# Kernel optimization log

Hardware: AMD Instinct MI355X
Metric: run time of the kernel (lower is better)

Reference implementation:

```python
import jax, jax.numpy as jnp
import numpy as np

B, S, D, DQK, DV = 4, 2048, 1024, 128, 256
EPS = 1e-8


def setup_inputs() -> dict:
    key = jax.random.key(0)
    ks = jax.random.split(key, 11)
    s = lambda fan_in: 1.0 / np.sqrt(fan_in)
    return {
        "X": jax.random.normal(ks[0], (B, S, D), dtype=jnp.float32),
        "Wq": jax.random.uniform(ks[1], (D, DQK), minval=-s(D), maxval=s(D), dtype=jnp.float32),
        "bq": jax.random.uniform(ks[2], (DQK,), minval=-s(D), maxval=s(D), dtype=jnp.float32),
        "Wk": jax.random.uniform(ks[3], (D, DQK), minval=-s(D), maxval=s(D), dtype=jnp.float32),
        "bk": jax.random.uniform(ks[4], (DQK,), minval=-s(D), maxval=s(D), dtype=jnp.float32),
        "Wv": jax.random.uniform(ks[5], (D, DV), minval=-s(D), maxval=s(D), dtype=jnp.float32),
        "bv": jax.random.uniform(ks[6], (DV,), minval=-s(D), maxval=s(D), dtype=jnp.float32),
        "Wg": jax.random.uniform(ks[7], (D, DV), minval=-s(D), maxval=s(D), dtype=jnp.float32),
        "bg": jax.random.uniform(ks[8], (DV,), minval=-s(D), maxval=s(D), dtype=jnp.float32),
        "Wp": jax.random.uniform(ks[9], (DV, D), minval=-s(DV), maxval=s(DV), dtype=jnp.float32),
        "bp": jax.random.uniform(ks[10], (D,), minval=-s(DV), maxval=s(DV), dtype=jnp.float32),
    }


def _shepards(Q, K, V, p=2, eps=EPS):
    # Euclidean cdist via ||q||^2 + ||k||^2 - 2 q.k  (then sqrt)
    q2 = jnp.sum(Q * Q, axis=-1, keepdims=True)          # [B,Sq,1]
    k2 = jnp.sum(K * K, axis=-1, keepdims=True)          # [B,Sk,1]
    d2 = q2 + jnp.swapaxes(k2, -1, -2) - 2.0 * jnp.einsum("bqd,bkd->bqk", Q, K)
    Dm = jnp.sqrt(jnp.maximum(d2, 0.0))                  # [B,Sq,Sk]
    W = jnp.power(jnp.maximum(Dm, eps), -float(p))
    A = W / jnp.sum(W, axis=2, keepdims=True)
    return jnp.einsum("bqk,bkv->bqv", A, V)


def reference(X, Wq, bq, Wk, bk, Wv, bv, Wg, bg, Wp, bp):
    N = X  # norm is Identity
    Q = N @ Wq + bq
    K = N @ Wk + bk
    V = N @ Wv + bv
    A = _shepards(Q, K, V)
    G = N @ Wg + bg
    return X + (A * G) @ Wp + bp
```

## Files before the change

kernel.cpp:

```cpp
#include <hip/hip_runtime.h>
#include <stdint.h>

#define SLEN 2048
#define NROWS 8192

typedef __attribute__((ext_vector_type(4))) float f32x4;
typedef __attribute__((ext_vector_type(8))) short bf16x8;

__device__ __forceinline__ short f2bf(float f) {
  uint32_t u = __builtin_bit_cast(uint32_t, f);
  u += 0x7FFFu + ((u >> 16) & 1u);
  return (short)(u >> 16);
}
__device__ __forceinline__ float bf2f(short s) {
  uint32_t u = ((uint32_t)(uint16_t)s) << 16;
  return __builtin_bit_cast(float, u);
}
__device__ __forceinline__ f32x4 mfma16(bf16x8 a, bf16x8 b, f32x4 c) {
  return __builtin_amdgcn_mfma_f32_16x16x32_bf16(a, b, c, 0, 0, 0);
}
__device__ __forceinline__ void gld_lds16(const void* g, void* l) {
  __builtin_amdgcn_global_load_lds(
      (const __attribute__((address_space(1))) void*)g,
      (__attribute__((address_space(3))) void*)l, 16, 0, 0);
}

__global__ __launch_bounds__(256) void k_prep(
    const float* __restrict__ X,
    const float* __restrict__ Wq, const float* __restrict__ bq,
    const float* __restrict__ Wk, const float* __restrict__ bk,
    const float* __restrict__ Wv, const float* __restrict__ bv,
    const float* __restrict__ Wg, const float* __restrict__ bg,
    const float* __restrict__ Wp,
    short* __restrict__ Xb, short* __restrict__ WcatT,
    short* __restrict__ WpT, float* __restrict__ bcat) {
  int blk = blockIdx.x, tid = threadIdx.x;
  if (blk < 4096) {
    size_t e = ((size_t)blk * 256 + tid) * 8;
    f32x4 a = *(const f32x4*)&X[e];
    f32x4 b = *(const f32x4*)&X[e + 4];
    bf16x8 o;
    o[0] = f2bf(a[0]); o[1] = f2bf(a[1]); o[2] = f2bf(a[2]); o[3] = f2bf(a[3]);
    o[4] = f2bf(b[0]); o[5] = f2bf(b[1]); o[6] = f2bf(b[2]); o[7] = f2bf(b[3]);
    *(bf16x8*)&Xb[e] = o;
  } else if (blk < 7168) {
    int flat = (blk - 4096) * 256 + tid;
    int c = flat >> 10, d = flat & 1023;
    float v;
    if (c < 128)      v = Wq[d * 128 + c];
    else if (c < 256) v = Wk[d * 128 + (c - 128)];
    else if (c < 512) v = Wv[d * 256 + (c - 256)];
    else              v = Wg[d * 256 + (c - 512)];
    WcatT[flat] = f2bf(v);
  } else if (blk < 8192) {
    int flat = (blk - 7168) * 256 + tid;
    int n = flat >> 8, k = flat & 255;
    WpT[flat] = f2bf(Wp[(size_t)k * 1024 + n]);
  } else {
    int c = (blk - 8192) * 256 + tid;
    if (c < 768) {
      float v;
      if (c < 128)      v = bq[c];
      else if (c < 256) v = bk[c - 128];
      else if (c < 512) v = bv[c - 256];
      else              v = bg[c - 512];
      bcat[c] = v;
    }
  }
}

__global__ __launch_bounds__(256) void k_gemm1(
    const short* __restrict__ Xb, const short* __restrict__ WcatT,
    const float* __restrict__ bcat, short* __restrict__ O) {
  __shared__ short At[128 * 32];
  __shared__ short Bt[128 * 32];
  const int tid = threadIdx.x;
  const int w = tid >> 6, l = tid & 63, lg = l >> 4, lc = l & 15;
  const int m0 = blockIdx.x * 128, n0 = blockIdx.y * 128;
  const int sr0 = w * 32 + (l >> 2);
  const int scc = (l & 3) * 8;
  const int wm = (w >> 1) * 64, wn = (w & 1) * 64;

  f32x4 acc[4][4] = {};
  const short* Ab = Xb + (size_t)m0 * 1024;
  const short* Bb = WcatT + (size_t)n0 * 1024;

  for (int kb = 0; kb < 1024; kb += 32) {
    gld_lds16(Ab + (size_t)sr0 * 1024 + kb + scc, &At[(w * 32) * 32]);
    gld_lds16(Ab + (size_t)(sr0 + 16) * 1024 + kb + scc, &At[(w * 32 + 16) * 32]);
    gld_lds16(Bb + (size_t)sr0 * 1024 + kb + scc, &Bt[(w * 32) * 32]);
    gld_lds16(Bb + (size_t)(sr0 + 16) * 1024 + kb + scc, &Bt[(w * 32 + 16) * 32]);
    __syncthreads();
    bf16x8 af[4], bf[4];
#pragma unroll
    for (int mi = 0; mi < 4; ++mi)
      af[mi] = *(const bf16x8*)&At[(wm + mi * 16 + lc) * 32 + lg * 8];
#pragma unroll
    for (int ni = 0; ni < 4; ++ni)
      bf[ni] = *(const bf16x8*)&Bt[(wn + ni * 16 + lc) * 32 + lg * 8];
#pragma unroll
    for (int mi = 0; mi < 4; ++mi)
#pragma unroll
      for (int ni = 0; ni < 4; ++ni)
        acc[mi][ni] = mfma16(af[mi], bf[ni], acc[mi][ni]);
    __syncthreads();
  }
#pragma unroll
  for (int mi = 0; mi < 4; ++mi) {
    int gr = m0 + wm + mi * 16 + lg * 4;
#pragma unroll
    for (int ni = 0; ni < 4; ++ni) {
      int gc = n0 + wn + ni * 16 + lc;
      float bias = bcat[gc];
#pragma unroll
      for (int r = 0; r < 4; ++r)
        O[(size_t)(gr + r) * 768 + gc] = f2bf(acc[mi][ni][r] + bias);
    }
  }
}

__global__ __launch_bounds__(256) void k_mid(
    const short* __restrict__ O, float* __restrict__ q2a,
    float* __restrict__ k2a, short* __restrict__ Vt) {
  __shared__ short tile[64][33];
  int blk = blockIdx.x, tid = threadIdx.x;
  if (blk < 4096) {
    int isK = blk >= 2048;
    int row = (blk & 2047) * 4 + (tid >> 6);
    int l = tid & 63;
    uint32_t u = *(const uint32_t*)&O[(size_t)row * 768 + (isK ? 128 : 0) + l * 2];
    float a = bf2f((short)(u & 0xFFFFu));
    float b = bf2f((short)(u >> 16));
    float s = a * a + b * b;
#pragma unroll
    for (int m = 1; m < 64; m <<= 1) s += __shfl_xor(s, m, 64);
    if (l == 0) (isK ? k2a : q2a)[row] = s;
  } else {
    int t = blk - 4096;
    int b = t >> 8, rem = t & 255;
    int s0 = (rem >> 3) * 64, dv0 = (rem & 7) * 32;
    int r = tid >> 2, cg = (tid & 3) * 8;
    bf16x8 v = *(const bf16x8*)&O[(size_t)(b * SLEN + s0 + r) * 768 + 256 + dv0 + cg];
#pragma unroll
    for (int j = 0; j < 8; ++j) tile[r][cg + j] = v[j];
    __syncthreads();
    int dr = tid >> 3, sg = (tid & 7) * 8;
    bf16x8 ov;
#pragma unroll
    for (int j = 0; j < 8; ++j) ov[j] = tile[sg + j][dr];
    *(bf16x8*)&Vt[(size_t)(b * 256 + dv0 + dr) * SLEN + s0 + sg] = ov;
  }
}

__global__ __launch_bounds__(256) void k_attn(
    const short* __restrict__ O, const short* __restrict__ Vt,
    const float* __restrict__ q2a, const float* __restrict__ k2a,
    short* __restrict__ nump, float* __restrict__ denp) {
  __shared__ short Wt[32 * 256];
  __shared__ float dls[4][32];
  const int tid = threadIdx.x;
  const int w = tid >> 6, l = tid & 63, lg = l >> 4, lc = l & 15;
  const int blk = blockIdx.x;
  const int ks = blk & 3;
  const int qt = (blk >> 2) & 63;
  const int b = blk >> 8;
  const int grow0 = b * SLEN + qt * 32;

  bf16x8 qf[2][4];
#pragma unroll
  for (int mi = 0; mi < 2; ++mi)
#pragma unroll
    for (int kf = 0; kf < 4; ++kf)
      qf[mi][kf] = *(const bf16x8*)&O[(size_t)(grow0 + mi * 16 + lc) * 768 + kf * 32 + lg * 8];

  float q2r[2][4];
#pragma unroll
  for (int mi = 0; mi < 2; ++mi)
#pragma unroll
    for (int r = 0; r < 4; ++r)
      q2r[mi][r] = q2a[grow0 + mi * 16 + lg * 4 + r];

  f32x4 acc[2][4] = {};
  float den[2][4] = {};

  for (int it = 0; it < 2; ++it) {
    const int kt = ks * 512 + it * 256;
    const int krow = b * SLEN + kt + w * 64;
    f32x4 s[2][4] = {};
#pragma unroll
    for (int nk = 0; nk < 4; ++nk) {
#pragma unroll
      for (int kf = 0; kf < 4; ++kf) {
        bf16x8 kv = *(const bf16x8*)&O[(size_t)(krow + nk * 16 + lc) * 768 + 128 + kf * 32 + lg * 8];
        s[0][nk] = mfma16(qf[0][kf], kv, s[0][nk]);
        s[1][nk] = mfma16(qf[1][kf], kv, s[1][nk]);
      }
    }
    float k2r[4];
#pragma unroll
    for (int nk = 0; nk < 4; ++nk) k2r[nk] = k2a[krow + nk * 16 + lc];
#pragma unroll
    for (int mi = 0; mi < 2; ++mi)
#pragma unroll
      for (int nk = 0; nk < 4; ++nk)
#pragma unroll
        for (int r = 0; r < 4; ++r) {
          float d2 = q2r[mi][r] + k2r[nk] - 2.0f * s[mi][nk][r];
          d2 = fmaxf(d2, 1e-16f);
          float wg = __builtin_amdgcn_rcpf(d2);
          den[mi][r] += wg;
          int rr = mi * 16 + lg * 4 + r;
          int byte = rr * 512 + (w * 64 + nk * 16 + lc) * 2;
          byte ^= (rr & 7) << 4;
          *(short*)((char*)Wt + byte) = f2bf(wg);
        }
    __syncthreads();
#pragma unroll
    for (int kf2 = 0; kf2 < 8; ++kf2) {
      bf16x8 af0, af1;
      {
        int rr = lc;
        int byte = rr * 512 + kf2 * 64 + lg * 16; byte ^= (rr & 7) << 4;
        af0 = *(const bf16x8*)((const char*)Wt + byte);
      }
      {
        int rr = 16 + lc;
        int byte = rr * 512 + kf2 * 64 + lg * 16; byte ^= (rr & 7) << 4;
        af1 = *(const bf16x8*)((const char*)Wt + byte);
      }
#pragma unroll
      for (int nv = 0; nv < 4; ++nv) {
        bf16x8 bv = *(const bf16x8*)&Vt[(size_t)(b * 256 + w * 64 + nv * 16 + lc) * SLEN + kt + kf2 * 32 + lg * 8];
        acc[0][nv] = mfma16(af0, bv, acc[0][nv]);
        acc[1][nv] = mfma16(af1, bv, acc[1][nv]);
      }
    }
    __syncthreads();
  }
#pragma unroll
  for (int mi = 0; mi < 2; ++mi)
#pragma unroll
    for (int r = 0; r < 4; ++r) {
      float v = den[mi][r];
      v += __shfl_xor(v, 1, 64); v += __shfl_xor(v, 2, 64);
      v += __shfl_xor(v, 4, 64); v += __shfl_xor(v, 8, 64);
      den[mi][r] = v;
    }
  if (lc == 0) {
#pragma unroll
    for (int mi = 0; mi < 2; ++mi)
#pragma unroll
      for (int r = 0; r < 4; ++r) dls[w][mi * 16 + lg * 4 + r] = den[mi][r];
  }
  __syncthreads();
  const size_t pbase = (size_t)blk * 32 * 256;
#pragma unroll
  for (int mi = 0; mi < 2; ++mi)
#pragma unroll
    for (int nv = 0; nv < 4; ++nv) {
      int dv = w * 64 + nv * 16 + lc;
#pragma unroll
      for (int r = 0; r < 4; ++r) {
        int rit = mi * 16 + lg * 4 + r;
        nump[pbase + (size_t)rit * 256 + dv] = f2bf(acc[mi][nv][r]);
      }
    }
  if (w == 0 && lc == 0) {
#pragma unroll
    for (int mi = 0; mi < 2; ++mi)
#pragma unroll
      for (int r = 0; r < 4; ++r) {
        int rit = mi * 16 + lg * 4 + r;
        denp[blk * 32 + rit] = dls[0][rit] + dls[1][rit] + dls[2][rit] + dls[3][rit];
      }
  }
}

__global__ __launch_bounds__(256) void k_red(
    const short* __restrict__ nump, const float* __restrict__ denp,
    const short* __restrict__ O, short* __restrict__ AG) {
  int flat = blockIdx.x * 256 + threadIdx.x;
  int idx8 = flat * 8;
  int row = idx8 >> 8;
  int dv0 = idx8 & 255;
  int b = row >> 11, srow = row & 2047;
  int qt = srow >> 5, rit = srow & 31;
  int blkbase = (b * 64 + qt) << 2;
  float num[8] = {};
  float den = 0.f;
#pragma unroll
  for (int ksi = 0; ksi < 4; ++ksi) {
    const size_t base = ((size_t)(blkbase + ksi) * 32 + rit) * 256 + dv0;
    bf16x8 v = *(const bf16x8*)&nump[base];
#pragma unroll
    for (int j = 0; j < 8; ++j) num[j] += bf2f(v[j]);
    den += denp[(blkbase + ksi) * 32 + rit];
  }
  float rden = 1.f / den;
  bf16x8 gv = *(const bf16x8*)&O[(size_t)row * 768 + 512 + dv0];
  bf16x8 o;
#pragma unroll
  for (int j = 0; j < 8; ++j) o[j] = f2bf(num[j] * rden * bf2f(gv[j]));
  *(bf16x8*)&AG[idx8] = o;
}

__global__ __launch_bounds__(256) void k_gemm3(
    const short* __restrict__ AG, const short* __restrict__ WpT,
    const float* __restrict__ X, const float* __restrict__ bp,
    float* __restrict__ Y) {
  __shared__ short At[128 * 32];
  __shared__ short Bt[128 * 32];
  const int tid = threadIdx.x;
  const int w = tid >> 6, l = tid & 63, lg = l >> 4, lc = l & 15;
  const int m0 = blockIdx.x * 128, n0 = blockIdx.y * 128;
  const int sr0 = w * 32 + (l >> 2);
  const int scc = (l & 3) * 8;
  const int wm = (w >> 1) * 64, wn = (w & 1) * 64;

  f32x4 acc[4][4] = {};
  const short* Ab = AG + (size_t)m0 * 256;
  const short* Bb = WpT + (size_t)n0 * 256;

  for (int kb = 0; kb < 256; kb += 32) {
    gld_lds16(Ab + (size_t)sr0 * 256 + kb + scc, &At[(w * 32) * 32]);
    gld_lds16(Ab + (size_t)(sr0 + 16) * 256 + kb + scc, &At[(w * 32 + 16) * 32]);
    gld_lds16(Bb + (size_t)sr0 * 256 + kb + scc, &Bt[(w * 32) * 32]);
    gld_lds16(Bb + (size_t)(sr0 + 16) * 256 + kb + scc, &Bt[(w * 32 + 16) * 32]);
    __syncthreads();
    bf16x8 af[4], bf[4];
#pragma unroll
    for (int mi = 0; mi < 4; ++mi)
      af[mi] = *(const bf16x8*)&At[(wm + mi * 16 + lc) * 32 + lg * 8];
#pragma unroll
    for (int ni = 0; ni < 4; ++ni)
      bf[ni] = *(const bf16x8*)&Bt[(wn + ni * 16 + lc) * 32 + lg * 8];
#pragma unroll
    for (int mi = 0; mi < 4; ++mi)
#pragma unroll
      for (int ni = 0; ni < 4; ++ni)
        acc[mi][ni] = mfma16(af[mi], bf[ni], acc[mi][ni]);
    __syncthreads();
  }
#pragma unroll
  for (int mi = 0; mi < 4; ++mi) {
    int gr = m0 + wm + mi * 16 + lg * 4;
#pragma unroll
    for (int ni = 0; ni < 4; ++ni) {
      int gc = n0 + wn + ni * 16 + lc;
      float bias = bp[gc];
#pragma unroll
      for (int r = 0; r < 4; ++r) {
        size_t idx = (size_t)(gr + r) * 1024 + gc;
        Y[idx] = acc[mi][ni][r] + X[idx] + bias;
      }
    }
  }
}

extern "C" void kernel_launch(void* const* d_in, const int* in_sizes, int n_in,
                              void* d_out, int out_size, void* d_ws, size_t ws_size,
                              hipStream_t stream) {
  const float* X  = (const float*)d_in[0];
  const float* Wq = (const float*)d_in[1];
  const float* bq = (const float*)d_in[2];
  const float* Wk = (const float*)d_in[3];
  const float* bk = (const float*)d_in[4];
  const float* Wv = (const float*)d_in[5];
  const float* bv = (const float*)d_in[6];
  const float* Wg = (const float*)d_in[7];
  const float* bg = (const float*)d_in[8];
  const float* Wp = (const float*)d_in[9];
  const float* bp = (const float*)d_in[10];

  char* ws = (char*)d_ws;
  short* Xb    = (short*)(ws + 0);
  short* WcatT = (short*)(ws + 16777216);
  short* WpT   = (short*)(ws + 18350080);
  float* bcat  = (float*)(ws + 18874368);
  short* O     = (short*)(ws + 18878464);
  short* Vt    = (short*)(ws + 31461376);
  float* q2a   = (float*)(ws + 35655680);
  float* k2a   = (float*)(ws + 35688448);
  short* AG    = (short*)(ws + 35721216);
  short* nump  = (short*)(ws + 0);
  float* denp  = (float*)(ws + 16777216);
  float* Y = (float*)d_out;

  hipLaunchKernelGGL(k_prep, dim3(8195), dim3(256), 0, stream,
                     X, Wq, bq, Wk, bk, Wv, bv, Wg, bg, Wp, Xb, WcatT, WpT, bcat);
  hipLaunchKernelGGL(k_gemm1, dim3(64, 6), dim3(256), 0, stream, Xb, WcatT, bcat, O);
  hipLaunchKernelGGL(k_mid, dim3(5120), dim3(256), 0, stream, O, q2a, k2a, Vt);
  hipLaunchKernelGGL(k_attn, dim3(1024), dim3(256), 0, stream, O, Vt, q2a, k2a, nump, denp);
  hipLaunchKernelGGL(k_red, dim3(1024), dim3(256), 0, stream, nump, denp, O, AG);
  hipLaunchKernelGGL(k_gemm3, dim3(64, 8), dim3(256), 0, stream, AG, WpT, X, bp, Y);
}
```

Measured before the change: 220.8 us.

## Fuse row norms into GEMM1, tile weight transposes, swap attention MFMA operands

```diff
diff --git a/kernel.cpp b/kernel.cpp
--- a/kernel.cpp
+++ b/kernel.cpp
@@ -6,6 +6,7 @@
 
 typedef __attribute__((ext_vector_type(4))) float f32x4;
 typedef __attribute__((ext_vector_type(8))) short bf16x8;
+typedef __attribute__((ext_vector_type(2))) unsigned int u32x2;
 
 __device__ __forceinline__ short f2bf(float f) {
   uint32_t u = __builtin_bit_cast(uint32_t, f);
@@ -34,6 +35,7 @@
     const float* __restrict__ Wp,
     short* __restrict__ Xb, short* __restrict__ WcatT,
     short* __restrict__ WpT, float* __restrict__ bcat) {
+  __shared__ short tl[64][72];
   int blk = blockIdx.x, tid = threadIdx.x;
   if (blk < 4096) {
     size_t e = ((size_t)blk * 256 + tid) * 8;
@@ -43,21 +45,31 @@
     o[0] = f2bf(a[0]); o[1] = f2bf(a[1]); o[2] = f2bf(a[2]); o[3] = f2bf(a[3]);
     o[4] = f2bf(b[0]); o[5] = f2bf(b[1]); o[6] = f2bf(b[2]); o[7] = f2bf(b[3]);
     *(bf16x8*)&Xb[e] = o;
-  } else if (blk < 7168) {
-    int flat = (blk - 4096) * 256 + tid;
-    int c = flat >> 10, d = flat & 1023;
-    float v;
-    if (c < 128)      v = Wq[d * 128 + c];
-    else if (c < 256) v = Wk[d * 128 + (c - 128)];
-    else if (c < 512) v = Wv[d * 256 + (c - 256)];
-    else              v = Wg[d * 256 + (c - 512)];
-    WcatT[flat] = f2bf(v);
-  } else if (blk < 8192) {
-    int flat = (blk - 7168) * 256 + tid;
-    int n = flat >> 8, k = flat & 255;
-    WpT[flat] = f2bf(Wp[(size_t)k * 1024 + n]);
+  } else if (blk < 4352) {
+    int t = blk - 4096;
+    const float* src; short* dst; int C, rowoff, dstC, r0, c0;
+    if (t < 32)       { src = Wq; C = 128;  rowoff = 0;   dst = WcatT; dstC = 1024; r0 = (t >> 1) * 64;  c0 = (t & 1) * 64; }
+    else if (t < 64)  { t -= 32;  src = Wk; C = 128;  rowoff = 128; dst = WcatT; dstC = 1024; r0 = (t >> 1) * 64;  c0 = (t & 1) * 64; }
+    else if (t < 128) { t -= 64;  src = Wv; C = 256;  rowoff = 256; dst = WcatT; dstC = 1024; r0 = (t >> 2) * 64;  c0 = (t & 3) * 64; }
+    else if (t < 192) { t -= 128; src = Wg; C = 256;  rowoff = 512; dst = WcatT; dstC = 1024; r0 = (t >> 2) * 64;  c0 = (t & 3) * 64; }
+    else              { t -= 192; src = Wp; C = 1024; rowoff = 0;   dst = WpT;   dstC = 256;  r0 = (t >> 4) * 64;  c0 = (t & 15) * 64; }
+    int lr = tid >> 4, lcc = tid & 15;
+#pragma unroll
+    for (int rr = 0; rr < 4; ++rr) {
+      f32x4 v = *(const f32x4*)&src[(size_t)(r0 + lr * 4 + rr) * C + c0 + lcc * 4];
+#pragma unroll
+      for (int j = 0; j < 4; ++j) tl[lcc * 4 + j][lr * 4 + rr] = f2bf(v[j]);
+    }
+    __syncthreads();
+    int orow = tid >> 2, og = (tid & 3) * 16;
+    bf16x8 o1, o2;
+#pragma unroll
+    for (int j = 0; j < 8; ++j) { o1[j] = tl[orow][og + j]; o2[j] = tl[orow][og + 8 + j]; }
+    size_t dbase = (size_t)(rowoff + c0 + orow) * dstC + r0 + og;
+    *(bf16x8*)&dst[dbase] = o1;
+    *(bf16x8*)&dst[dbase + 8] = o2;
   } else {
-    int c = (blk - 8192) * 256 + tid;
+    int c = tid;
     if (c < 768) {
       float v;
       if (c < 128)      v = bq[c];
@@ -71,9 +83,11 @@
 
 __global__ __launch_bounds__(256) void k_gemm1(
     const short* __restrict__ Xb, const short* __restrict__ WcatT,
-    const float* __restrict__ bcat, short* __restrict__ O) {
+    const float* __restrict__ bcat, short* __restrict__ O,
+    float* __restrict__ q2a, float* __restrict__ k2a) {
   __shared__ short At[128 * 32];
   __shared__ short Bt[128 * 32];
+  __shared__ float nlds[128][2];
   const int tid = threadIdx.x;
   const int w = tid >> 6, l = tid & 63, lg = l >> 4, lc = l & 15;
   const int m0 = blockIdx.x * 128, n0 = blockIdx.y * 128;
@@ -105,6 +119,7 @@
         acc[mi][ni] = mfma16(af[mi], bf[ni], acc[mi][ni]);
     __syncthreads();
   }
+  float sq[4][4] = {};
 #pragma unroll
   for (int mi = 0; mi < 4; ++mi) {
     int gr = m0 + wm + mi * 16 + lg * 4;
@@ -113,43 +128,55 @@
       int gc = n0 + wn + ni * 16 + lc;
       float bias = bcat[gc];
 #pragma unroll
-      for (int r = 0; r < 4; ++r)
-        O[(size_t)(gr + r) * 768 + gc] = f2bf(acc[mi][ni][r] + bias);
-    }
-  }
-}
-
-__global__ __launch_bounds__(256) void k_mid(
-    const short* __restrict__ O, float* __restrict__ q2a,
-    float* __restrict__ k2a, short* __restrict__ Vt) {
+      for (int r = 0; r < 4; ++r) {
+        short sv = f2bf(acc[mi][ni][r] + bias);
+        O[(size_t)(gr + r) * 768 + gc] = sv;
+        float v = bf2f(sv);
+        sq[mi][r] += v * v;
+      }
+    }
+  }
+  if (blockIdx.y < 2) {
+#pragma unroll
+    for (int mi = 0; mi < 4; ++mi)
+#pragma unroll
+      for (int r = 0; r < 4; ++r) {
+        float v = sq[mi][r];
+        v += __shfl_xor(v, 1, 64); v += __shfl_xor(v, 2, 64);
+        v += __shfl_xor(v, 4, 64); v += __shfl_xor(v, 8, 64);
+        sq[mi][r] = v;
+      }
+    if (lc == 0) {
+#pragma unroll
+      for (int mi = 0; mi < 4; ++mi)
+#pragma unroll
+        for (int r = 0; r < 4; ++r)
+          nlds[wm + mi * 16 + lg * 4 + r][w & 1] = sq[mi][r];
+    }
+    __syncthreads();
+    if (tid < 128) {
+      float t = nlds[tid][0] + nlds[tid][1];
+      (blockIdx.y == 0 ? q2a : k2a)[m0 + tid] = t;
+    }
+  }
+}
+
+__global__ __launch_bounds__(256) void k_vt(
+    const short* __restrict__ O, short* __restrict__ Vt) {
   __shared__ short tile[64][33];
   int blk = blockIdx.x, tid = threadIdx.x;
-  if (blk < 4096) {
-    int isK = blk >= 2048;
-    int row = (blk & 2047) * 4 + (tid >> 6);
-    int l = tid & 63;
-    uint32_t u = *(const uint32_t*)&O[(size_t)row * 768 + (isK ? 128 : 0) + l * 2];
-    float a = bf2f((short)(u & 0xFFFFu));
-    float b = bf2f((short)(u >> 16));
-    float s = a * a + b * b;
-#pragma unroll
-    for (int m = 1; m < 64; m <<= 1) s += __shfl_xor(s, m, 64);
-    if (l == 0) (isK ? k2a : q2a)[row] = s;
-  } else {
-    int t = blk - 4096;
-    int b = t >> 8, rem = t & 255;
-    int s0 = (rem >> 3) * 64, dv0 = (rem & 7) * 32;
-    int r = tid >> 2, cg = (tid & 3) * 8;
-    bf16x8 v = *(const bf16x8*)&O[(size_t)(b * SLEN + s0 + r) * 768 + 256 + dv0 + cg];
-#pragma unroll
-    for (int j = 0; j < 8; ++j) tile[r][cg + j] = v[j];
-    __syncthreads();
-    int dr = tid >> 3, sg = (tid & 7) * 8;
-    bf16x8 ov;
-#pragma unroll
-    for (int j = 0; j < 8; ++j) ov[j] = tile[sg + j][dr];
-    *(bf16x8*)&Vt[(size_t)(b * 256 + dv0 + dr) * SLEN + s0 + sg] = ov;
-  }
+  int b = blk >> 8, rem = blk & 255;
+  int s0 = (rem >> 3) * 64, dv0 = (rem & 7) * 32;
+  int r = tid >> 2, cg = (tid & 3) * 8;
+  bf16x8 v = *(const bf16x8*)&O[(size_t)(b * SLEN + s0 + r) * 768 + 256 + dv0 + cg];
+#pragma unroll
+  for (int j = 0; j < 8; ++j) tile[r][cg + j] = v[j];
+  __syncthreads();
+  int dr = tid >> 3, sg = (tid & 7) * 8;
+  bf16x8 ov;
+#pragma unroll
+  for (int j = 0; j < 8; ++j) ov[j] = tile[sg + j][dr];
+  *(bf16x8*)&Vt[(size_t)(b * 256 + dv0 + dr) * SLEN + s0 + sg] = ov;
 }
 
 __global__ __launch_bounds__(256) void k_attn(
@@ -160,7 +187,7 @@
   __shared__ float dls[4][32];
   const int tid = threadIdx.x;
   const int w = tid >> 6, l = tid & 63, lg = l >> 4, lc = l & 15;
-  const int blk = blockIdx.x;
+  const int blk = ((blockIdx.x & 7) << 7) | (blockIdx.x >> 3);
   const int ks = blk & 3;
   const int qt = (blk >> 2) & 63;
   const int b = blk >> 8;
@@ -173,15 +200,12 @@
     for (int kf = 0; kf < 4; ++kf)
       qf[mi][kf] = *(const bf16x8*)&O[(size_t)(grow0 + mi * 16 + lc) * 768 + kf * 32 + lg * 8];
 
-  float q2r[2][4];
-#pragma unroll
-  for (int mi = 0; mi < 2; ++mi)
-#pragma unroll
-    for (int r = 0; r < 4; ++r)
-      q2r[mi][r] = q2a[grow0 + mi * 16 + lg * 4 + r];
+  float q2s[2];
+  q2s[0] = q2a[grow0 + lc];
+  q2s[1] = q2a[grow0 + 16 + lc];
 
   f32x4 acc[2][4] = {};
-  float den[2][4] = {};
+  float den0 = 0.f, den1 = 0.f;
 
   for (int it = 0; it < 2; ++it) {
     const int kt = ks * 512 + it * 256;
@@ -192,28 +216,36 @@
 #pragma unroll
       for (int kf = 0; kf < 4; ++kf) {
         bf16x8 kv = *(const bf16x8*)&O[(size_t)(krow + nk * 16 + lc) * 768 + 128 + kf * 32 + lg * 8];
-        s[0][nk] = mfma16(qf[0][kf], kv, s[0][nk]);
-        s[1][nk] = mfma16(qf[1][kf], kv, s[1][nk]);
-      }
-    }
-    float k2r[4];
-#pragma unroll
-    for (int nk = 0; nk < 4; ++nk) k2r[nk] = k2a[krow + nk * 16 + lc];
-#pragma unroll
-    for (int mi = 0; mi < 2; ++mi)
-#pragma unroll
-      for (int nk = 0; nk < 4; ++nk)
+        s[0][nk] = mfma16(kv, qf[0][kf], s[0][nk]);
+        s[1][nk] = mfma16(kv, qf[1][kf], s[1][nk]);
+      }
+    }
+#pragma unroll
+    for (int nk = 0; nk < 4; ++nk) {
+      f32x4 k2v = *(const f32x4*)&k2a[krow + nk * 16 + lg * 4];
+      float wv[2][4];
+#pragma unroll
+      for (int mi = 0; mi < 2; ++mi)
 #pragma unroll
         for (int r = 0; r < 4; ++r) {
-          float d2 = q2r[mi][r] + k2r[nk] - 2.0f * s[mi][nk][r];
+          float d2 = q2s[mi] + k2v[r] - 2.0f * s[mi][nk][r];
           d2 = fmaxf(d2, 1e-16f);
-          float wg = __builtin_amdgcn_rcpf(d2);
-          den[mi][r] += wg;
-          int rr = mi * 16 + lg * 4 + r;
-          int byte = rr * 512 + (w * 64 + nk * 16 + lc) * 2;
-          byte ^= (rr & 7) << 4;
-          *(short*)((char*)Wt + byte) = f2bf(wg);
+          wv[mi][r] = __builtin_amdgcn_rcpf(d2);
         }
+      den0 += wv[0][0] + wv[0][1] + wv[0][2] + wv[0][3];
+      den1 += wv[1][0] + wv[1][1] + wv[1][2] + wv[1][3];
+      int col = w * 64 + nk * 16 + lg * 4;
+#pragma unroll
+      for (int mi = 0; mi < 2; ++mi) {
+        u32x2 pk;
+        pk[0] = (uint32_t)(uint16_t)f2bf(wv[mi][0]) | ((uint32_t)(uint16_t)f2bf(wv[mi][1]) << 16);
+        pk[1] = (uint32_t)(uint16_t)f2bf(wv[mi][2]) | ((uint32_t)(uint16_t)f2bf(wv[mi][3]) << 16);
+        int q = mi * 16 + lc;
+        int byte = q * 512 + col * 2;
+        byte ^= (q & 7) << 4;
+        *(u32x2*)((char*)Wt + byte) = pk;
+      }
+    }
     __syncthreads();
 #pragma unroll
     for (int kf2 = 0; kf2 < 8; ++kf2) {
@@ -237,21 +269,9 @@
     }
     __syncthreads();
   }
-#pragma unroll
-  for (int mi = 0; mi < 2; ++mi)
-#pragma unroll
-    for (int r = 0; r < 4; ++r) {
-      float v = den[mi][r];
-      v += __shfl_xor(v, 1, 64); v += __shfl_xor(v, 2, 64);
-      v += __shfl_xor(v, 4, 64); v += __shfl_xor(v, 8, 64);
-      den[mi][r] = v;
-    }
-  if (lc == 0) {
-#pragma unroll
-    for (int mi = 0; mi < 2; ++mi)
-#pragma unroll
-      for (int r = 0; r < 4; ++r) dls[w][mi * 16 + lg * 4 + r] = den[mi][r];
-  }
+  den0 += __shfl_xor(den0, 16, 64); den0 += __shfl_xor(den0, 32, 64);
+  den1 += __shfl_xor(den1, 16, 64); den1 += __shfl_xor(den1, 32, 64);
+  if (l < 16) { dls[w][lc] = den0; dls[w][16 + lc] = den1; }
   __syncthreads();
   const size_t pbase = (size_t)blk * 32 * 256;
 #pragma unroll
@@ -265,15 +285,8 @@
         nump[pbase + (size_t)rit * 256 + dv] = f2bf(acc[mi][nv][r]);
       }
     }
-  if (w == 0 && lc == 0) {
-#pragma unroll
-    for (int mi = 0; mi < 2; ++mi)
-#pragma unroll
-      for (int r = 0; r < 4; ++r) {
-        int rit = mi * 16 + lg * 4 + r;
-        denp[blk * 32 + rit] = dls[0][rit] + dls[1][rit] + dls[2][rit] + dls[3][rit];
-      }
-  }
+  if (tid < 32)
+    denp[blk * 32 + tid] = dls[0][tid] + dls[1][tid] + dls[2][tid] + dls[3][tid];
 }
 
 __global__ __launch_bounds__(256) void k_red(
@@ -386,10 +399,10 @@
   float* denp  = (float*)(ws + 16777216);
   float* Y = (float*)d_out;
 
-  hipLaunchKernelGGL(k_prep, dim3(8195), dim3(256), 0, stream,
+  hipLaunchKernelGGL(k_prep, dim3(4353), dim3(256), 0, stream,
                      X, Wq, bq, Wk, bk, Wv, bv, Wg, bg, Wp, Xb, WcatT, WpT, bcat);
-  hipLaunchKernelGGL(k_gemm1, dim3(64, 6), dim3(256), 0, stream, Xb, WcatT, bcat, O);
-  hipLaunchKernelGGL(k_mid, dim3(5120), dim3(256), 0, stream, O, q2a, k2a, Vt);
+  hipLaunchKernelGGL(k_gemm1, dim3(64, 6), dim3(256), 0, stream, Xb, WcatT, bcat, O, q2a, k2a);
+  hipLaunchKernelGGL(k_vt, dim3(1024), dim3(256), 0, stream, O, Vt);
   hipLaunchKernelGGL(k_attn, dim3(1024), dim3(256), 0, stream, O, Vt, q2a, k2a, nump, denp);
   hipLaunchKernelGGL(k_red, dim3(1024), dim3(256), 0, stream, nump, denp, O, AG);
   hipLaunchKernelGGL(k_gemm3, dim3(64, 8), dim3(256), 0, stream, AG, WpT, X, bp, Y);
```

New measurement: 214.3 us. -2.9%, faster.
